# Performance work log

Measured on AMD Instinct MI355X. Metric: run time of the kernel, lower is better.

## Reference

```python
import jax, jax.numpy as jnp
import numpy as np

B, T, E, H = 256, 128, 300, 2048


def setup_inputs() -> dict:
    key = jax.random.key(0)
    k0, k1, k2, k3, k4 = jax.random.split(key, 5)
    s = 1.0 / np.sqrt(H)  # PyTorch LSTM init range
    return {
        "x": jax.random.normal(k0, (B, T, E), dtype=jnp.float32),
        "W_ih": jax.random.uniform(k1, (4 * H, E), dtype=jnp.float32, minval=-s, maxval=s),
        "W_hh": jax.random.uniform(k2, (4 * H, H), dtype=jnp.float32, minval=-s, maxval=s),
        "b_ih": jax.random.uniform(k3, (4 * H,), dtype=jnp.float32, minval=-s, maxval=s),
        "b_hh": jax.random.uniform(k4, (4 * H,), dtype=jnp.float32, minval=-s, maxval=s),
    }


def reference(x, W_ih, W_hh, b_ih, b_hh):
    # x: [B, T, E]; returns final hidden state h_T: [B, H]
    Bn = x.shape[0]
    Hn = W_hh.shape[1]
    # Precompute input-to-gate projection for all timesteps: [B, T, 4H]
    x_gates = jnp.einsum('bte,ge->btg', x, W_ih) + b_ih + b_hh

    def step(carry, xg_t):
        h, c = carry
        gates = xg_t + h @ W_hh.T  # [B, 4H]
        i, f, g, o = jnp.split(gates, 4, axis=-1)  # PyTorch gate order i,f,g,o
        i = jax.nn.sigmoid(i)
        f = jax.nn.sigmoid(f)
        g = jnp.tanh(g)
        o = jax.nn.sigmoid(o)
        c = f * c + i * g
        h = o * jnp.tanh(c)
        return (h, c), None

    h0 = jnp.zeros((Bn, Hn), dtype=x.dtype)
    c0 = jnp.zeros((Bn, Hn), dtype=x.dtype)
    (h_T, _), _ = jax.lax.scan(step, (h0, c0), jnp.swapaxes(x_gates, 0, 1))
    return h_T
```

## Files before the change

### kernel.cpp

```cpp
#include <hip/hip_runtime.h>

typedef unsigned short u16;
typedef unsigned int u32;
typedef __bf16 bf16x8 __attribute__((ext_vector_type(8)));
typedef float f32x4 __attribute__((ext_vector_type(4)));

#define B_ 256
#define T_ 128
#define E_ 300
#define EP 320
#define H_ 2048
#define G_ 8192

#define OFF_XBF   0UL
#define OFF_WIH   20971520UL
#define OFF_WHH   26214400UL
#define OFF_BIAS  59768832UL
#define OFF_HBUF  59801600UL
#define OFF_BAR   61898752UL

#define GLDS16(gp, sp)                                                    \
  __builtin_amdgcn_global_load_lds(                                       \
      (__attribute__((address_space(1))) void*)(void*)(gp),               \
      (__attribute__((address_space(3))) void*)(sp), 16, 0, 0)
#define GLDS16C(gp, sp)                                                   \
  __builtin_amdgcn_global_load_lds(                                       \
      (__attribute__((address_space(1))) void*)(void*)(gp),               \
      (__attribute__((address_space(3))) void*)(sp), 16, 0, 17)

__device__ __forceinline__ u16 f2bf(float f) {
  u32 u = __builtin_bit_cast(u32, f);
  return (u16)((u + 0x7FFFu + ((u >> 16) & 1u)) >> 16);
}
__device__ __forceinline__ float sigm_f(float x) {
  return __builtin_amdgcn_rcpf(1.0f + __expf(-x));
}
__device__ __forceinline__ float tanh_f(float x) {
  return 1.0f - 2.0f * __builtin_amdgcn_rcpf(1.0f + __expf(2.0f * x));
}

__global__ void prep_kernel(const float* __restrict__ x, const float* __restrict__ Wih,
                            const float* __restrict__ Whh, const float* __restrict__ bih,
                            const float* __restrict__ bhh, u16* __restrict__ xbf,
                            u16* __restrict__ wihb, u16* __restrict__ whhb,
                            float* __restrict__ biasc, u32* __restrict__ bar) {
  const long NX = (long)T_ * B_ * EP;
  const long NWIH = (long)G_ * EP;
  const long NWHH = (long)G_ * H_;
  const long NBS = G_;
  const long NBAR = T_;
  const long total = NX + NWIH + NWHH + NBS + NBAR;
  for (long q = (long)blockIdx.x * blockDim.x + threadIdx.x; q < total;
       q += (long)gridDim.x * blockDim.x) {
    long r = q;
    if (r < NX) {
      int t = (int)(r / (B_ * EP));
      int rem = (int)(r % (B_ * EP));
      int b = rem / EP, e = rem % EP;
      float v = (e < E_) ? x[((long)b * T_ + t) * E_ + e] : 0.0f;
      xbf[r] = f2bf(v);
    } else if ((r -= NX) < NWIH) {
      int n = (int)(r / EP), e = (int)(r % EP);
      wihb[r] = f2bf((e < E_) ? Wih[(long)n * E_ + e] : 0.0f);
    } else if ((r -= NWIH) < NWHH) {
      whhb[r] = f2bf(Whh[r]);
    } else if ((r -= NWHH) < NBS) {
      biasc[r] = bih[r] + bhh[r];
    } else {
      r -= NBS;
      bar[r] = 0;
    }
  }
}

__global__ void __launch_bounds__(256, 1)
lstm_kernel(const u16* __restrict__ xbf, const u16* __restrict__ wihb,
            const u16* __restrict__ whhb, const float* __restrict__ biasc,
            u16* __restrict__ hbuf, u32* __restrict__ bar, float* __restrict__ out) {
  __shared__ __align__(16) u16 As[4][64 * 64];
  __shared__ __align__(16) u16 Bs[4][128 * 64];

  const int tid = threadIdx.x;
  const int l = tid & 63;
  const int w = tid >> 6;
  const int wr = w >> 1, wj = w & 1;
  const int bid = blockIdx.x;
  const int b0 = (bid >> 6) << 6;
  const int j0 = (bid & 63) << 5;
  const int jc = j0 + (wj << 4) + (l & 15);
  const int cgl = (tid & 7) ^ ((tid >> 3) & 7);

  const float bi = biasc[jc];
  const float bff = biasc[2048 + jc];
  const float bg = biasc[4096 + jc];
  const float bo = biasc[6144 + jc];

  float cst[2][4];
#pragma unroll
  for (int mi = 0; mi < 2; ++mi)
#pragma unroll
    for (int r = 0; r < 4; ++r) cst[mi][r] = 0.0f;

  auto stageA = [&](const u16* srcA, int strA, int kk, int p, bool coh) {
    u16* Ad = &As[p][w * 512];
#pragma unroll
    for (int i = 0; i < 2; ++i) {
      int slot = i * 256 + tid;
      const u16* g = srcA + (size_t)(slot >> 3) * strA + kk + cgl * 8;
      if (coh) { GLDS16C(g, Ad + i * 2048); } else { GLDS16(g, Ad + i * 2048); }
    }
  };
  auto stageB = [&](const u16* srcB, int strB, int kk, int p) {
    u16* Bd = &Bs[p][w * 512];
#pragma unroll
    for (int i = 0; i < 4; ++i) {
      int slot = i * 256 + tid;
      int nl = slot >> 3;
      int grow = ((nl >> 5) << 11) + j0 + (nl & 31);
      const u16* g = srcB + (size_t)grow * strB + kk + cgl * 8;
      GLDS16(g, Bd + i * 2048);
    }
  };

  auto lead = [&](int vm) {
    switch (vm) {
      case 18: asm volatile("s_waitcnt vmcnt(18)" ::: "memory"); break;
      case 14: asm volatile("s_waitcnt vmcnt(14)" ::: "memory"); break;
      case 12: asm volatile("s_waitcnt vmcnt(12)" ::: "memory"); break;
      case 10: asm volatile("s_waitcnt vmcnt(10)" ::: "memory"); break;
      case 6:  asm volatile("s_waitcnt vmcnt(6)"  ::: "memory"); break;
      default: asm volatile("s_waitcnt vmcnt(0)"  ::: "memory"); break;
    }
    __builtin_amdgcn_s_barrier();
    __builtin_amdgcn_sched_barrier(0);
  };
  auto trail = [&]() {
    asm volatile("s_waitcnt lgkmcnt(0)" ::: "memory");
    __builtin_amdgcn_sched_barrier(0);
    __builtin_amdgcn_s_barrier();
  };

#pragma unroll 1
  for (int t = 0; t < T_; ++t) {
    const u16* hcur = hbuf + (size_t)(t & 1) * (B_ * H_) + (size_t)b0 * H_;
    u16* hnxt = hbuf + (size_t)((t + 1) & 1) * (B_ * H_);
    const u16* xsrc = xbf + (size_t)t * (B_ * EP) + (size_t)b0 * EP;

    f32x4 acc[2][4];
#pragma unroll
    for (int mi = 0; mi < 2; ++mi)
#pragma unroll
      for (int g = 0; g < 4; ++g) acc[mi][g] = (f32x4){0.f, 0.f, 0.f, 0.f};

    auto compute = [&](int p) {
#pragma unroll
      for (int k2 = 0; k2 < 2; ++k2) {
        int cp = ((k2 << 2) + (l >> 4)) ^ (l & 7);
        const u16* ap = &As[p][((wr << 5) + (l & 15)) * 64 + cp * 8];
        bf16x8 a0 = *(const bf16x8*)ap;
        bf16x8 a1 = *(const bf16x8*)(ap + 1024);
        const u16* bp = &Bs[p][((wj << 4) + (l & 15)) * 64 + cp * 8];
        bf16x8 bv0 = *(const bf16x8*)bp;
        bf16x8 bv1 = *(const bf16x8*)(bp + 2048);
        bf16x8 bv2 = *(const bf16x8*)(bp + 4096);
        bf16x8 bv3 = *(const bf16x8*)(bp + 6144);
        acc[0][0] = __builtin_amdgcn_mfma_f32_16x16x32_bf16(a0, bv0, acc[0][0], 0, 0, 0);
        acc[0][1] = __builtin_amdgcn_mfma_f32_16x16x32_bf16(a0, bv1, acc[0][1], 0, 0, 0);
        acc[0][2] = __builtin_amdgcn_mfma_f32_16x16x32_bf16(a0, bv2, acc[0][2], 0, 0, 0);
        acc[0][3] = __builtin_amdgcn_mfma_f32_16x16x32_bf16(a0, bv3, acc[0][3], 0, 0, 0);
        acc[1][0] = __builtin_amdgcn_mfma_f32_16x16x32_bf16(a1, bv0, acc[1][0], 0, 0, 0);
        acc[1][1] = __builtin_amdgcn_mfma_f32_16x16x32_bf16(a1, bv1, acc[1][1], 0, 0, 0);
        acc[1][2] = __builtin_amdgcn_mfma_f32_16x16x32_bf16(a1, bv2, acc[1][2], 0, 0, 0);
        acc[1][3] = __builtin_amdgcn_mfma_f32_16x16x32_bf16(a1, bv3, acc[1][3], 0, 0, 0);
      }
    };

    stageA(xsrc, EP, 0, 0, false);   stageB(wihb, EP, 0, 0);
    stageA(xsrc, EP, 64, 1, false);  stageB(wihb, EP, 64, 1);
    stageA(xsrc, EP, 128, 2, false); stageB(wihb, EP, 128, 2);
    stageA(xsrc, EP, 192, 3, false); stageB(wihb, EP, 192, 3);
    lead(18); compute(0); trail();
    stageA(xsrc, EP, 256, 0, false); stageB(wihb, EP, 256, 0);
    lead(18); compute(1); trail();
    lead(12); compute(2); trail();
    lead(6);  compute(3); trail();
    lead(0);  compute(0); trail();

    if (t > 0) {
      stageB(whhb, H_, 0, 0);
      stageB(whhb, H_, 64, 1);
      stageB(whhb, H_, 128, 2);
      if (tid == 0) {
        while (__hip_atomic_load(&bar[t - 1], __ATOMIC_RELAXED,
                                 __HIP_MEMORY_SCOPE_AGENT) < 256u)
          __builtin_amdgcn_s_sleep(2);
      }
      __syncthreads();
      stageA(hcur, H_, 0, 0, true);
      stageA(hcur, H_, 64, 1, true);
      stageA(hcur, H_, 128, 2, true);
#pragma unroll 1
      for (int kh = 0; kh < 32; ++kh) {
        if (kh < 29) {
          stageA(hcur, H_, (kh + 3) << 6, (kh + 3) & 3, true);
          stageB(whhb, H_, (kh + 3) << 6, (kh + 3) & 3);
        }
        int vm = (kh == 0) ? 10 : (kh == 1) ? 14 : (kh < 29) ? 18 : (31 - kh) * 6;
        lead(vm);
        compute(kh & 3);
        trail();
      }
    }

#pragma unroll
    for (int mi = 0; mi < 2; ++mi) {
#pragma unroll
      for (int r = 0; r < 4; ++r) {
        float ig = sigm_f(acc[mi][0][r] + bi);
        float fg = sigm_f(acc[mi][1][r] + bff);
        float gg = tanh_f(acc[mi][2][r] + bg);
        float og = sigm_f(acc[mi][3][r] + bo);
        float c = fg * cst[mi][r] + ig * gg;
        cst[mi][r] = c;
        float h = og * tanh_f(c);
        int row = b0 + (wr << 5) + (mi << 4) + ((l >> 4) << 2) + r;
        if (t < T_ - 1) {
          u16 hv = f2bf(h);
          u16* hp = hnxt + (size_t)row * H_ + jc;
          asm volatile("global_store_short %0, %1, off sc0 sc1"
                       :: "v"(hp), "v"((u32)hv) : "memory");
        } else {
          out[(size_t)row * H_ + jc] = h;
        }
      }
    }

    if (t < T_ - 1) {
      __builtin_amdgcn_s_waitcnt(0);
      __syncthreads();
      if (tid == 0)
        __hip_atomic_fetch_add(&bar[t], 1u, __ATOMIC_RELAXED,
                               __HIP_MEMORY_SCOPE_AGENT);
    }
  }
}

extern "C" void kernel_launch(void* const* d_in, const int* in_sizes, int n_in,
                              void* d_out, int out_size, void* d_ws, size_t ws_size,
                              hipStream_t stream) {
  const float* x = (const float*)d_in[0];
  const float* Wih = (const float*)d_in[1];
  const float* Whh = (const float*)d_in[2];
  const float* bih = (const float*)d_in[3];
  const float* bhh = (const float*)d_in[4];
  char* ws = (char*)d_ws;
  u16* xbf = (u16*)(ws + OFF_XBF);
  u16* wihb = (u16*)(ws + OFF_WIH);
  u16* whhb = (u16*)(ws + OFF_WHH);
  float* biasc = (float*)(ws + OFF_BIAS);
  u16* hbuf = (u16*)(ws + OFF_HBUF);
  u32* bar = (u32*)(ws + OFF_BAR);
  float* out = (float*)d_out;

  hipLaunchKernelGGL(prep_kernel, dim3(2048), dim3(256), 0, stream,
                     x, Wih, Whh, bih, bhh, xbf, wihb, whhb, biasc, bar);

  void* args[] = {(void*)&xbf, (void*)&wihb, (void*)&whhb,
                  (void*)&biasc, (void*)&hbuf, (void*)&bar, (void*)&out};
  hipLaunchCooperativeKernel((void*)lstm_kernel, dim3(256), dim3(256), args, 0, stream);
}
```

Before: 3.728 ms.

## Double threads per block to 512 so each wave computes one M-tile

```diff
diff --git a/kernel.cpp b/kernel.cpp
--- a/kernel.cpp
+++ b/kernel.cpp
@@ -73,7 +73,7 @@
   }
 }
 
-__global__ void __launch_bounds__(256, 1)
+__global__ void __launch_bounds__(512, 2)
 lstm_kernel(const u16* __restrict__ xbf, const u16* __restrict__ wihb,
             const u16* __restrict__ whhb, const float* __restrict__ biasc,
             u16* __restrict__ hbuf, u32* __restrict__ bar, float* __restrict__ out) {
@@ -95,41 +95,35 @@
   const float bg = biasc[4096 + jc];
   const float bo = biasc[6144 + jc];
 
-  float cst[2][4];
-#pragma unroll
-  for (int mi = 0; mi < 2; ++mi)
-#pragma unroll
-    for (int r = 0; r < 4; ++r) cst[mi][r] = 0.0f;
+  float cst[4];
+#pragma unroll
+  for (int r = 0; r < 4; ++r) cst[r] = 0.0f;
 
   auto stageA = [&](const u16* srcA, int strA, int kk, int p, bool coh) {
     u16* Ad = &As[p][w * 512];
-#pragma unroll
-    for (int i = 0; i < 2; ++i) {
-      int slot = i * 256 + tid;
-      const u16* g = srcA + (size_t)(slot >> 3) * strA + kk + cgl * 8;
-      if (coh) { GLDS16C(g, Ad + i * 2048); } else { GLDS16(g, Ad + i * 2048); }
-    }
+    const u16* g = srcA + (size_t)(tid >> 3) * strA + kk + cgl * 8;
+    if (coh) { GLDS16C(g, Ad); } else { GLDS16(g, Ad); }
   };
   auto stageB = [&](const u16* srcB, int strB, int kk, int p) {
     u16* Bd = &Bs[p][w * 512];
 #pragma unroll
-    for (int i = 0; i < 4; ++i) {
-      int slot = i * 256 + tid;
+    for (int i = 0; i < 2; ++i) {
+      int slot = i * 512 + tid;
       int nl = slot >> 3;
       int grow = ((nl >> 5) << 11) + j0 + (nl & 31);
       const u16* g = srcB + (size_t)grow * strB + kk + cgl * 8;
-      GLDS16(g, Bd + i * 2048);
+      GLDS16(g, Bd + i * 4096);
     }
   };
 
   auto lead = [&](int vm) {
     switch (vm) {
-      case 18: asm volatile("s_waitcnt vmcnt(18)" ::: "memory"); break;
-      case 14: asm volatile("s_waitcnt vmcnt(14)" ::: "memory"); break;
-      case 12: asm volatile("s_waitcnt vmcnt(12)" ::: "memory"); break;
-      case 10: asm volatile("s_waitcnt vmcnt(10)" ::: "memory"); break;
-      case 6:  asm volatile("s_waitcnt vmcnt(6)"  ::: "memory"); break;
-      default: asm volatile("s_waitcnt vmcnt(0)"  ::: "memory"); break;
+      case 9: asm volatile("s_waitcnt vmcnt(9)" ::: "memory"); break;
+      case 7: asm volatile("s_waitcnt vmcnt(7)" ::: "memory"); break;
+      case 6: asm volatile("s_waitcnt vmcnt(6)" ::: "memory"); break;
+      case 5: asm volatile("s_waitcnt vmcnt(5)" ::: "memory"); break;
+      case 3: asm volatile("s_waitcnt vmcnt(3)" ::: "memory"); break;
+      default: asm volatile("s_waitcnt vmcnt(0)" ::: "memory"); break;
     }
     __builtin_amdgcn_s_barrier();
     __builtin_amdgcn_sched_barrier(0);
@@ -146,32 +140,25 @@
     u16* hnxt = hbuf + (size_t)((t + 1) & 1) * (B_ * H_);
     const u16* xsrc = xbf + (size_t)t * (B_ * EP) + (size_t)b0 * EP;
 
-    f32x4 acc[2][4];
-#pragma unroll
-    for (int mi = 0; mi < 2; ++mi)
-#pragma unroll
-      for (int g = 0; g < 4; ++g) acc[mi][g] = (f32x4){0.f, 0.f, 0.f, 0.f};
+    f32x4 acc[4];
+#pragma unroll
+    for (int g = 0; g < 4; ++g) acc[g] = (f32x4){0.f, 0.f, 0.f, 0.f};
 
     auto compute = [&](int p) {
 #pragma unroll
       for (int k2 = 0; k2 < 2; ++k2) {
         int cp = ((k2 << 2) + (l >> 4)) ^ (l & 7);
-        const u16* ap = &As[p][((wr << 5) + (l & 15)) * 64 + cp * 8];
+        const u16* ap = &As[p][((wr << 4) + (l & 15)) * 64 + cp * 8];
         bf16x8 a0 = *(const bf16x8*)ap;
-        bf16x8 a1 = *(const bf16x8*)(ap + 1024);
         const u16* bp = &Bs[p][((wj << 4) + (l & 15)) * 64 + cp * 8];
         bf16x8 bv0 = *(const bf16x8*)bp;
         bf16x8 bv1 = *(const bf16x8*)(bp + 2048);
         bf16x8 bv2 = *(const bf16x8*)(bp + 4096);
         bf16x8 bv3 = *(const bf16x8*)(bp + 6144);
-        acc[0][0] = __builtin_amdgcn_mfma_f32_16x16x32_bf16(a0, bv0, acc[0][0], 0, 0, 0);
-        acc[0][1] = __builtin_amdgcn_mfma_f32_16x16x32_bf16(a0, bv1, acc[0][1], 0, 0, 0);
-        acc[0][2] = __builtin_amdgcn_mfma_f32_16x16x32_bf16(a0, bv2, acc[0][2], 0, 0, 0);
-        acc[0][3] = __builtin_amdgcn_mfma_f32_16x16x32_bf16(a0, bv3, acc[0][3], 0, 0, 0);
-        acc[1][0] = __builtin_amdgcn_mfma_f32_16x16x32_bf16(a1, bv0, acc[1][0], 0, 0, 0);
-        acc[1][1] = __builtin_amdgcn_mfma_f32_16x16x32_bf16(a1, bv1, acc[1][1], 0, 0, 0);
-        acc[1][2] = __builtin_amdgcn_mfma_f32_16x16x32_bf16(a1, bv2, acc[1][2], 0, 0, 0);
-        acc[1][3] = __builtin_amdgcn_mfma_f32_16x16x32_bf16(a1, bv3, acc[1][3], 0, 0, 0);
+        acc[0] = __builtin_amdgcn_mfma_f32_16x16x32_bf16(a0, bv0, acc[0], 0, 0, 0);
+        acc[1] = __builtin_amdgcn_mfma_f32_16x16x32_bf16(a0, bv1, acc[1], 0, 0, 0);
+        acc[2] = __builtin_amdgcn_mfma_f32_16x16x32_bf16(a0, bv2, acc[2], 0, 0, 0);
+        acc[3] = __builtin_amdgcn_mfma_f32_16x16x32_bf16(a0, bv3, acc[3], 0, 0, 0);
       }
     };
 
@@ -179,12 +166,12 @@
     stageA(xsrc, EP, 64, 1, false);  stageB(wihb, EP, 64, 1);
     stageA(xsrc, EP, 128, 2, false); stageB(wihb, EP, 128, 2);
     stageA(xsrc, EP, 192, 3, false); stageB(wihb, EP, 192, 3);
-    lead(18); compute(0); trail();
+    lead(9); compute(0); trail();
     stageA(xsrc, EP, 256, 0, false); stageB(wihb, EP, 256, 0);
-    lead(18); compute(1); trail();
-    lead(12); compute(2); trail();
-    lead(6);  compute(3); trail();
-    lead(0);  compute(0); trail();
+    lead(9); compute(1); trail();
+    lead(6); compute(2); trail();
+    lead(3); compute(3); trail();
+    lead(0); compute(0); trail();
 
     if (t > 0) {
       stageB(whhb, H_, 0, 0);
@@ -205,7 +192,8 @@
           stageA(hcur, H_, (kh + 3) << 6, (kh + 3) & 3, true);
           stageB(whhb, H_, (kh + 3) << 6, (kh + 3) & 3);
         }
-        int vm = (kh == 0) ? 10 : (kh == 1) ? 14 : (kh < 29) ? 18 : (31 - kh) * 6;
+        int vm = (kh == 0) ? 5 : (kh == 1) ? 7 : (kh < 29) ? 9
+               : (kh == 29) ? 6 : (kh == 30) ? 3 : 0;
         lead(vm);
         compute(kh & 3);
         trail();
@@ -213,25 +201,22 @@
     }
 
 #pragma unroll
-    for (int mi = 0; mi < 2; ++mi) {
-#pragma unroll
-      for (int r = 0; r < 4; ++r) {
-        float ig = sigm_f(acc[mi][0][r] + bi);
-        float fg = sigm_f(acc[mi][1][r] + bff);
-        float gg = tanh_f(acc[mi][2][r] + bg);
-        float og = sigm_f(acc[mi][3][r] + bo);
-        float c = fg * cst[mi][r] + ig * gg;
-        cst[mi][r] = c;
-        float h = og * tanh_f(c);
-        int row = b0 + (wr << 5) + (mi << 4) + ((l >> 4) << 2) + r;
-        if (t < T_ - 1) {
-          u16 hv = f2bf(h);
-          u16* hp = hnxt + (size_t)row * H_ + jc;
-          asm volatile("global_store_short %0, %1, off sc0 sc1"
-                       :: "v"(hp), "v"((u32)hv) : "memory");
-        } else {
-          out[(size_t)row * H_ + jc] = h;
-        }
+    for (int r = 0; r < 4; ++r) {
+      float ig = sigm_f(acc[0][r] + bi);
+      float fg = sigm_f(acc[1][r] + bff);
+      float gg = tanh_f(acc[2][r] + bg);
+      float og = sigm_f(acc[3][r] + bo);
+      float c = fg * cst[r] + ig * gg;
+      cst[r] = c;
+      float h = og * tanh_f(c);
+      int row = b0 + (wr << 4) + ((l >> 4) << 2) + r;
+      if (t < T_ - 1) {
+        u16 hv = f2bf(h);
+        u16* hp = hnxt + (size_t)row * H_ + jc;
+        asm volatile("global_store_short %0, %1, off sc0 sc1"
+                     :: "v"(hp), "v"((u32)hv) : "memory");
+      } else {
+        out[(size_t)row * H_ + jc] = h;
       }
     }
 
@@ -267,5 +252,5 @@
 
   void* args[] = {(void*)&xbf, (void*)&wihb, (void*)&whhb,
                   (void*)&biasc, (void*)&hbuf, (void*)&bar, (void*)&out};
-  hipLaunchCooperativeKernel((void*)lstm_kernel, dim3(256), dim3(256), args, 0, stream);
-}
+  hipLaunchCooperativeKernel((void*)lstm_kernel, dim3(256), dim3(512), args, 0, stream);
+}
```

After: 3.629 ms. 1.03x faster.
